# Kernel optimization log

Measured on AMD Instinct MI355X. Metric: run time of the kernel, lower is better.

## Reference

```python
import jax, jax.numpy as jnp
import numpy as np


def setup_inputs() -> dict:
    key = jax.random.key(0)
    k1, k2, k3, k4 = jax.random.split(key, 4)
    B, S, d_in, d_out = 4, 2048, 1024, 1024
    x = jax.random.normal(k1, (B, S, d_in), dtype=jnp.float32)
    # torch nn.Linear weight is [d_out, d_in]; we store transposed [d_in, d_out]
    Wq = jax.random.normal(k2, (d_in, d_out), dtype=jnp.float32) * (1.0 / np.sqrt(d_in))
    Wk = jax.random.normal(k3, (d_in, d_out), dtype=jnp.float32) * (1.0 / np.sqrt(d_in))
    Wv = jax.random.normal(k4, (d_in, d_out), dtype=jnp.float32) * (1.0 / np.sqrt(d_in))
    return {"x": x, "Wq": Wq, "Wk": Wk, "Wv": Wv}


def reference(x, Wq, Wk, Wv):
    # x: [B, S, d_in]
    B, S, d_in = x.shape
    q = jnp.einsum("bsd,de->bse", x, Wq)
    k = jnp.einsum("bsd,de->bse", x, Wk)
    v = jnp.einsum("bsd,de->bse", x, Wv)
    scores = jnp.einsum("bqe,bke->bqk", q, k)  # [B, S, S]
    causal = jnp.triu(jnp.ones((S, S), dtype=bool), k=1)  # True above diagonal
    scores = jnp.where(causal[None, :, :], -jnp.inf, scores)
    # NOTE: original scales by sqrt(d_in), not sqrt(d_out)
    scale = jnp.asarray(1.0 / np.sqrt(d_in), dtype=scores.dtype)
    weights = jax.nn.softmax(scores * scale, axis=-1)
    # dropout p=0.0 -> identity
    return jnp.einsum("bqk,bke->bqe", weights, v)
```

## Files before the change

kernel.cpp:

```cpp
#include <hip/hip_runtime.h>
#include <hip/hip_bf16.h>

typedef __attribute__((ext_vector_type(8))) short short8;
typedef __attribute__((ext_vector_type(4))) float f32x4;
typedef unsigned short ushort_t;

__device__ __forceinline__ ushort_t f2bf(float f) {
    union { __hip_bfloat16 h; ushort_t u; } c;
    c.h = __float2bfloat16(f);
    return c.u;
}

__device__ __forceinline__ void gload16(const ushort_t* g, ushort_t* l) {
    __builtin_amdgcn_global_load_lds(
        (const __attribute__((address_space(1))) void*)g,
        (__attribute__((address_space(3))) void*)l, 16, 0, 0);
}

__global__ __launch_bounds__(256) void k_convert_x(const float* __restrict__ x,
                                                   ushort_t* __restrict__ xb) {
    size_t idx = ((size_t)blockIdx.x * 256 + threadIdx.x) * 8;
    float4 a = *(const float4*)(x + idx);
    float4 b = *(const float4*)(x + idx + 4);
    short8 o;
    o[0] = (short)f2bf(a.x); o[1] = (short)f2bf(a.y);
    o[2] = (short)f2bf(a.z); o[3] = (short)f2bf(a.w);
    o[4] = (short)f2bf(b.x); o[5] = (short)f2bf(b.y);
    o[6] = (short)f2bf(b.z); o[7] = (short)f2bf(b.w);
    *(short8*)(xb + idx) = o;
}

__global__ __launch_bounds__(256) void k_transpose_w(const float* __restrict__ W0,
                                                     const float* __restrict__ W1,
                                                     const float* __restrict__ W2,
                                                     ushort_t* __restrict__ Wt) {
    const float* W = (blockIdx.z == 0) ? W0 : (blockIdx.z == 1) ? W1 : W2;
    ushort_t* out = Wt + (size_t)blockIdx.z * 1024 * 1024;
    __shared__ float tile[32][33];
    int tx = threadIdx.x, ty = threadIdx.y;
    int d0 = blockIdx.y * 32, e0 = blockIdx.x * 32;
#pragma unroll
    for (int i = 0; i < 32; i += 8)
        tile[ty + i][tx] = W[(size_t)(d0 + ty + i) * 1024 + e0 + tx];
    __syncthreads();
#pragma unroll
    for (int i = 0; i < 32; i += 8)
        out[(size_t)(e0 + ty + i) * 1024 + d0 + tx] = f2bf(tile[tx][ty + i]);
}

__global__ __launch_bounds__(256) void k_transpose_v(const ushort_t* __restrict__ V,
                                                     ushort_t* __restrict__ Vt) {
    int b = blockIdx.z;
    const ushort_t* in = V + (size_t)b * 2048 * 1024;
    ushort_t* out = Vt + (size_t)b * 1024 * 2048;
    __shared__ ushort_t tile[32][33];
    int tx = threadIdx.x, ty = threadIdx.y;
    int e0 = blockIdx.x * 32, j0 = blockIdx.y * 32;
#pragma unroll
    for (int i = 0; i < 32; i += 8)
        tile[ty + i][tx] = in[(size_t)(j0 + ty + i) * 1024 + e0 + tx];
    __syncthreads();
#pragma unroll
    for (int i = 0; i < 32; i += 8)
        out[(size_t)(e0 + ty + i) * 2048 + j0 + tx] = tile[tx][ty + i];
}

__global__ __launch_bounds__(512) void k_proj256(const ushort_t* __restrict__ X,
                                                 const ushort_t* __restrict__ Wt,
                                                 ushort_t* __restrict__ QKV) {
    const int bm = blockIdx.x, bn = blockIdx.y;

    __shared__ ushort_t Asm[2][16384];
    __shared__ ushort_t Bsm[2][16384];

    const int tid = threadIdx.x;
    const int l = tid & 63, w = tid >> 6;
    const int wrow = w >> 2, wcol = w & 3;
    const int lr = l & 15, lg = l >> 4;
    const int cx = (lr & 7) << 3;

    const int srow = tid >> 3;
    const int scol = (((tid & 7) ^ (srow & 7)) << 3);
    const ushort_t* Ag = X  + (size_t)(bm * 256 + srow) * 1024 + scol;
    const ushort_t* Bg = Wt + (size_t)(bn * 256 + srow) * 1024 + scol;

    f32x4 zero = {0.f, 0.f, 0.f, 0.f};
    f32x4 acc[8][4];
#pragma unroll
    for (int m = 0; m < 8; ++m)
#pragma unroll
        for (int n = 0; n < 4; ++n) acc[m][n] = zero;

    auto stageA = [&](int T) {
        ushort_t* dst = &Asm[T & 1][tid * 8];
        const ushort_t* src = Ag + T * 64;
#pragma unroll
        for (int c = 0; c < 4; ++c)
            gload16(src + (size_t)(c * 64) * 1024, dst + c * 4096);
    };
    auto stageB = [&](int T) {
        ushort_t* dst = &Bsm[T & 1][tid * 8];
        const ushort_t* src = Bg + T * 64;
#pragma unroll
        for (int c = 0; c < 4; ++c)
            gload16(src + (size_t)(c * 64) * 1024, dst + c * 4096);
    };

    stageA(0); stageB(0);
    asm volatile("s_waitcnt vmcnt(0)" ::: "memory");
    __builtin_amdgcn_s_barrier();

    for (int T = 0; T < 16; ++T) {
        const ushort_t* As = Asm[T & 1];
        const ushort_t* Bs = Bsm[T & 1];
        short8 a[4][2], b[4][2];

        if (T + 1 < 16) stageA(T + 1);
#pragma unroll
        for (int nf = 0; nf < 4; ++nf)
#pragma unroll
            for (int kh = 0; kh < 2; ++kh)
                b[nf][kh] = *(const short8*)&Bs[(wcol * 64 + nf * 16 + lr) * 64 + ((kh * 32 + lg * 8) ^ cx)];
#pragma unroll
        for (int mf = 0; mf < 4; ++mf)
#pragma unroll
            for (int kh = 0; kh < 2; ++kh)
                a[mf][kh] = *(const short8*)&As[(wrow * 128 + mf * 16 + lr) * 64 + ((kh * 32 + lg * 8) ^ cx)];
        __builtin_amdgcn_s_setprio(1);
#pragma unroll
        for (int mf = 0; mf < 4; ++mf)
#pragma unroll
            for (int nf = 0; nf < 2; ++nf)
#pragma unroll
                for (int kh = 0; kh < 2; ++kh)
                    acc[mf][nf] = __builtin_amdgcn_mfma_f32_16x16x32_bf16(a[mf][kh], b[nf][kh], acc[mf][nf], 0, 0, 0);
        __builtin_amdgcn_s_setprio(0);
        __builtin_amdgcn_s_barrier();

        if (T + 1 < 16) stageB(T + 1);
        __builtin_amdgcn_s_setprio(1);
#pragma unroll
        for (int mf = 0; mf < 4; ++mf)
#pragma unroll
            for (int nf = 2; nf < 4; ++nf)
#pragma unroll
                for (int kh = 0; kh < 2; ++kh)
                    acc[mf][nf] = __builtin_amdgcn_mfma_f32_16x16x32_bf16(a[mf][kh], b[nf][kh], acc[mf][nf], 0, 0, 0);
        __builtin_amdgcn_s_setprio(0);
        __builtin_amdgcn_s_barrier();

#pragma unroll
        for (int mf = 0; mf < 4; ++mf)
#pragma unroll
            for (int kh = 0; kh < 2; ++kh)
                a[mf][kh] = *(const short8*)&As[(wrow * 128 + 64 + mf * 16 + lr) * 64 + ((kh * 32 + lg * 8) ^ cx)];
        __builtin_amdgcn_s_setprio(1);
#pragma unroll
        for (int mf = 0; mf < 4; ++mf)
#pragma unroll
            for (int nf = 0; nf < 2; ++nf)
#pragma unroll
                for (int kh = 0; kh < 2; ++kh)
                    acc[4 + mf][nf] = __builtin_amdgcn_mfma_f32_16x16x32_bf16(a[mf][kh], b[nf][kh], acc[4 + mf][nf], 0, 0, 0);
        __builtin_amdgcn_s_setprio(0);
        __builtin_amdgcn_s_barrier();

        __builtin_amdgcn_s_setprio(1);
#pragma unroll
        for (int mf = 0; mf < 4; ++mf)
#pragma unroll
            for (int nf = 2; nf < 4; ++nf)
#pragma unroll
                for (int kh = 0; kh < 2; ++kh)
                    acc[4 + mf][nf] = __builtin_amdgcn_mfma_f32_16x16x32_bf16(a[mf][kh], b[nf][kh], acc[4 + mf][nf], 0, 0, 0);
        __builtin_amdgcn_s_setprio(0);
        asm volatile("s_waitcnt vmcnt(0)" ::: "memory");
        __builtin_amdgcn_s_barrier();
    }

    ushort_t* C = QKV + (size_t)(bn >> 2) * 8388608;
    const int colbase = (bn & 3) * 256 + wcol * 64;
    const int rb = lg * 4;
#pragma unroll
    for (int m = 0; m < 8; ++m)
#pragma unroll
        for (int nf = 0; nf < 4; ++nf) {
            int col = colbase + nf * 16 + lr;
#pragma unroll
            for (int r = 0; r < 4; ++r) {
                int grow = bm * 256 + wrow * 128 + m * 16 + rb + r;
                C[(size_t)grow * 1024 + col] = f2bf(acc[m][nf][r]);
            }
        }
}

template <int MODE>
__global__ __launch_bounds__(256) void k_gemm(const ushort_t* __restrict__ Abase,
                                              const ushort_t* __restrict__ Bbase,
                                              void* __restrict__ Cbase) {
    const int bz = blockIdx.z;
    int bm, bn;
    const ushort_t* A;
    const ushort_t* B;
    int lda, ldb, nk;
    if constexpr (MODE == 1) {
        int x = blockIdx.x;
        bm = (int)((sqrtf(8.f * x + 1.f) - 1.f) * 0.5f);
        while ((bm + 1) * (bm + 2) / 2 <= x) ++bm;
        while (bm * (bm + 1) / 2 > x) --bm;
        bn = x - bm * (bm + 1) / 2;
        A = Abase + (size_t)bz * 2048 * 1024; lda = 1024;
        B = Bbase + (size_t)bz * 2048 * 1024; ldb = 1024;
        nk = 32;
    } else {
        int xr = blockIdx.x;
        bm = (xr & 1) ? (15 - (xr >> 1)) : (xr >> 1);
        bn = blockIdx.y;
        A = Abase + (size_t)bz * 2048 * 4096; lda = 4096;
        B = Bbase + (size_t)bz * 1024 * 2048; ldb = 2048;
        nk = (bm + 1) * 4;
    }

    __shared__ ushort_t As[128 * 32];
    __shared__ ushort_t Bs[128 * 32];

    const int tid = threadIdx.x;
    const int l = tid & 63, wid = tid >> 6;
    const int wr = (wid >> 1) * 64, wc = (wid & 1) * 64;
    const int lr = l & 15, kc = (l >> 4) * 8;

    const int srow = tid >> 2, skb = (tid & 3) * 8;
    const ushort_t* ag = A + (size_t)(bm * 128 + srow) * lda + skb;
    const ushort_t* bg = B + (size_t)(bn * 128 + srow) * ldb + skb;
    const size_t a64 = (size_t)64 * lda, b64 = (size_t)64 * ldb;
    ushort_t* al = As + tid * 8;
    ushort_t* bl = Bs + tid * 8;

    f32x4 zero = {0.f, 0.f, 0.f, 0.f};
    f32x4 acc[4][4];
#pragma unroll
    for (int m = 0; m < 4; ++m)
#pragma unroll
        for (int n = 0; n < 4; ++n) acc[m][n] = zero;

    for (int ks = 0; ks < nk; ++ks) {
        __syncthreads();
        gload16(ag, al);
        gload16(ag + a64, al + 2048);
        gload16(bg, bl);
        gload16(bg + b64, bl + 2048);
        ag += 32; bg += 32;
        __syncthreads();

        short8 a[4], b[4];
#pragma unroll
        for (int m = 0; m < 4; ++m)
            a[m] = *(const short8*)&As[(wr + m * 16 + lr) * 32 + kc];
#pragma unroll
        for (int n = 0; n < 4; ++n)
            b[n] = *(const short8*)&Bs[(wc + n * 16 + lr) * 32 + kc];
#pragma unroll
        for (int m = 0; m < 4; ++m)
#pragma unroll
            for (int n = 0; n < 4; ++n)
                acc[m][n] = __builtin_amdgcn_mfma_f32_16x16x32_bf16(a[m], b[n], acc[m][n], 0, 0, 0);
    }

    const int rbase = (l >> 4) * 4;
    const int cbase = l & 15;
#pragma unroll
    for (int m = 0; m < 4; ++m) {
#pragma unroll
        for (int n = 0; n < 4; ++n) {
            int row0 = wr + m * 16 + rbase;
            int col = wc + n * 16 + cbase;
            int gcol = bn * 128 + col;
#pragma unroll
            for (int r = 0; r < 4; ++r) {
                int grow = bm * 128 + row0 + r;
                float v = acc[m][n][r];
                if constexpr (MODE == 1) {
                    float* C = (float*)Cbase + (size_t)bz * 2048 * 2048;
                    if (gcol <= grow) C[(size_t)grow * 2048 + gcol] = v * 0.03125f;
                } else {
                    float* C = (float*)Cbase + (size_t)bz * 2048 * 1024;
                    C[(size_t)grow * 1024 + gcol] = v;
                }
            }
        }
    }
}

__global__ __launch_bounds__(256) void k_softmax(float* __restrict__ scores) {
    const int t = blockIdx.x;
    const int i = t & 2047;
    const int limit = ((i >> 7) + 1) << 7;
    float* row = scores + (size_t)t * 2048;
    const int tid = threadIdx.x;
    const int j0 = tid * 8;
    const bool active = (j0 < limit);

    float v[8];
    if (active) {
        float4 f0 = *(const float4*)(row + j0);
        float4 f1 = *(const float4*)(row + j0 + 4);
        v[0] = f0.x; v[1] = f0.y; v[2] = f0.z; v[3] = f0.w;
        v[4] = f1.x; v[5] = f1.y; v[6] = f1.z; v[7] = f1.w;
    }

    float m = -3.0e38f;
    if (active) {
#pragma unroll
        for (int e = 0; e < 8; ++e)
            if (j0 + e <= i) m = fmaxf(m, v[e]);
    }
#pragma unroll
    for (int off = 32; off > 0; off >>= 1) m = fmaxf(m, __shfl_down(m, off, 64));

    __shared__ float redm[4];
    __shared__ float reds[4];
    const int lane = tid & 63, wid = tid >> 6;
    if (lane == 0) redm[wid] = m;
    __syncthreads();
    m = fmaxf(fmaxf(redm[0], redm[1]), fmaxf(redm[2], redm[3]));

    float p[8];
    float s = 0.f;
    if (active) {
#pragma unroll
        for (int e = 0; e < 8; ++e) {
            p[e] = (j0 + e <= i) ? __expf(v[e] - m) : 0.f;
            s += p[e];
        }
    }
#pragma unroll
    for (int off = 32; off > 0; off >>= 1) s += __shfl_down(s, off, 64);
    if (lane == 0) reds[wid] = s;
    __syncthreads();
    s = reds[0] + reds[1] + reds[2] + reds[3];
    float inv = 1.f / s;

    if (active) {
        short8 o;
#pragma unroll
        for (int e = 0; e < 8; ++e) o[e] = (short)f2bf(p[e] * inv);
        *(short8*)((ushort_t*)row + j0) = o;
    }
}

extern "C" void kernel_launch(void* const* d_in, const int* in_sizes, int n_in,
                              void* d_out, int out_size, void* d_ws, size_t ws_size,
                              hipStream_t stream) {
    const float* x  = (const float*)d_in[0];
    const float* Wq = (const float*)d_in[1];
    const float* Wk = (const float*)d_in[2];
    const float* Wv = (const float*)d_in[3];

    char* ws = (char*)d_ws;
    ushort_t* xb     = (ushort_t*)(ws);
    ushort_t* Wt     = (ushort_t*)(ws + 16777216);
    ushort_t* QKV    = (ushort_t*)(ws + 23068672);
    ushort_t* Vt     = (ushort_t*)(ws + 73400320);
    float*    scores = (float*)   (ws + 90177536);

    ushort_t* Q = QKV;
    ushort_t* K = QKV + (size_t)8192 * 1024;
    ushort_t* V = QKV + (size_t)2 * 8192 * 1024;

    k_convert_x<<<4096, 256, 0, stream>>>(x, xb);
    k_transpose_w<<<dim3(32, 32, 3), dim3(32, 8), 0, stream>>>(Wq, Wk, Wv, Wt);
    k_proj256<<<dim3(32, 12), 512, 0, stream>>>(xb, Wt, QKV);
    k_transpose_v<<<dim3(32, 64, 4), dim3(32, 8), 0, stream>>>(V, Vt);
    k_gemm<1><<<dim3(136, 1, 4), 256, 0, stream>>>(Q, K, scores);
    k_softmax<<<8192, 256, 0, stream>>>(scores);
    k_gemm<2><<<dim3(16, 8, 4), 256, 0, stream>>>((const ushort_t*)scores, Vt, (float*)d_out);
}
```

Before: 204.2 us.

## Pipeline projection GEMM at half-tile granularity with deeper prefetch

Splits the shared-memory A/B tiles of the QKV projection GEMM into half-tiles and stages them at finer granularity. Each half-tile load is issued between MFMA phases, with the A half for step t+2 prefetched early, and the full vmcnt(0) drain is replaced by vmcnt(2). Warps now read from their own half-tile, and the loop is unrolled by 2 with explicit LDS waits and scheduling barriers. The goal is to overlap global-to-LDS traffic with matrix math and cut stalls at barriers. In exchange it adds more barriers and relies on delicate waitcnt accounting, where a miscount could race.

```diff
diff --git a/kernel.cpp b/kernel.cpp
--- a/kernel.cpp
+++ b/kernel.cpp
@@ -16,6 +16,8 @@
         (const __attribute__((address_space(1))) void*)g,
         (__attribute__((address_space(3))) void*)l, 16, 0, 0);
 }
+
+#define FENCE asm volatile("" ::: "memory")
 
 __global__ __launch_bounds__(256) void k_convert_x(const float* __restrict__ x,
                                                    ushort_t* __restrict__ xb) {
@@ -70,8 +72,8 @@
                                                  ushort_t* __restrict__ QKV) {
     const int bm = blockIdx.x, bn = blockIdx.y;
 
-    __shared__ ushort_t Asm[2][16384];
-    __shared__ ushort_t Bsm[2][16384];
+    __shared__ ushort_t Asm[2][2][8192];
+    __shared__ ushort_t Bsm[2][2][8192];
 
     const int tid = threadIdx.x;
     const int l = tid & 63, w = tid >> 6;
@@ -81,8 +83,21 @@
 
     const int srow = tid >> 3;
     const int scol = (((tid & 7) ^ (srow & 7)) << 3);
-    const ushort_t* Ag = X  + (size_t)(bm * 256 + srow) * 1024 + scol;
-    const ushort_t* Bg = Wt + (size_t)(bn * 256 + srow) * 1024 + scol;
+    const ushort_t* Ags = X  + (size_t)(bm * 256 + srow) * 1024 + scol;
+    const ushort_t* Bgs = Wt + (size_t)(bn * 256 + srow) * 1024 + scol;
+
+    auto stageA = [&](int T, int hf) {
+        const ushort_t* src = Ags + (size_t)(hf * 128) * 1024 + T * 64;
+        ushort_t* dst = &Asm[T & 1][hf][tid * 8];
+        gload16(src, dst);
+        gload16(src + (size_t)64 * 1024, dst + 4096);
+    };
+    auto stageB = [&](int T, int hf) {
+        const ushort_t* src = Bgs + (size_t)(hf * 128) * 1024 + T * 64;
+        ushort_t* dst = &Bsm[T & 1][hf][tid * 8];
+        gload16(src, dst);
+        gload16(src + (size_t)64 * 1024, dst + 4096);
+    };
 
     f32x4 zero = {0.f, 0.f, 0.f, 0.f};
     f32x4 acc[8][4];
@@ -91,41 +106,33 @@
 #pragma unroll
         for (int n = 0; n < 4; ++n) acc[m][n] = zero;
 
-    auto stageA = [&](int T) {
-        ushort_t* dst = &Asm[T & 1][tid * 8];
-        const ushort_t* src = Ag + T * 64;
-#pragma unroll
-        for (int c = 0; c < 4; ++c)
-            gload16(src + (size_t)(c * 64) * 1024, dst + c * 4096);
-    };
-    auto stageB = [&](int T) {
-        ushort_t* dst = &Bsm[T & 1][tid * 8];
-        const ushort_t* src = Bg + T * 64;
-#pragma unroll
-        for (int c = 0; c < 4; ++c)
-            gload16(src + (size_t)(c * 64) * 1024, dst + c * 4096);
-    };
-
-    stageA(0); stageB(0);
-    asm volatile("s_waitcnt vmcnt(0)" ::: "memory");
+    stageA(0, 0); stageB(0, 0); stageA(0, 1); stageB(0, 1); stageA(1, 0);
+    asm volatile("s_waitcnt vmcnt(2)" ::: "memory");
     __builtin_amdgcn_s_barrier();
 
-    for (int T = 0; T < 16; ++T) {
-        const ushort_t* As = Asm[T & 1];
-        const ushort_t* Bs = Bsm[T & 1];
-        short8 a[4][2], b[4][2];
-
-        if (T + 1 < 16) stageA(T + 1);
-#pragma unroll
-        for (int nf = 0; nf < 4; ++nf)
+    const int brow = (wcol & 1) * 64;
+
+#pragma unroll 2
+    for (int t = 0; t < 16; ++t) {
+        const int db = t & 1;
+        const ushort_t* Ah = Asm[db][wrow];
+        const ushort_t* Bh = Bsm[db][wcol >> 1];
+        short8 a[4][2], b0[2][2], b1[2][2];
+
+#pragma unroll
+        for (int mf = 0; mf < 4; ++mf)
 #pragma unroll
             for (int kh = 0; kh < 2; ++kh)
-                b[nf][kh] = *(const short8*)&Bs[(wcol * 64 + nf * 16 + lr) * 64 + ((kh * 32 + lg * 8) ^ cx)];
-#pragma unroll
-        for (int mf = 0; mf < 4; ++mf)
+                a[mf][kh] = *(const short8*)&Ah[(mf * 16 + lr) * 64 + ((kh * 32 + lg * 8) ^ cx)];
+#pragma unroll
+        for (int nf = 0; nf < 2; ++nf)
 #pragma unroll
             for (int kh = 0; kh < 2; ++kh)
-                a[mf][kh] = *(const short8*)&As[(wrow * 128 + mf * 16 + lr) * 64 + ((kh * 32 + lg * 8) ^ cx)];
+                b0[nf][kh] = *(const short8*)&Bh[(brow + nf * 16 + lr) * 64 + ((kh * 32 + lg * 8) ^ cx)];
+        if (t < 15) stageB(t + 1, 0);
+        FENCE; __builtin_amdgcn_s_barrier();
+        asm volatile("s_waitcnt lgkmcnt(0)" ::: "memory");
+        __builtin_amdgcn_sched_barrier(0);
         __builtin_amdgcn_s_setprio(1);
 #pragma unroll
         for (int mf = 0; mf < 4; ++mf)
@@ -133,27 +140,39 @@
             for (int nf = 0; nf < 2; ++nf)
 #pragma unroll
                 for (int kh = 0; kh < 2; ++kh)
-                    acc[mf][nf] = __builtin_amdgcn_mfma_f32_16x16x32_bf16(a[mf][kh], b[nf][kh], acc[mf][nf], 0, 0, 0);
+                    acc[mf][nf] = __builtin_amdgcn_mfma_f32_16x16x32_bf16(a[mf][kh], b0[nf][kh], acc[mf][nf], 0, 0, 0);
         __builtin_amdgcn_s_setprio(0);
-        __builtin_amdgcn_s_barrier();
-
-        if (T + 1 < 16) stageB(T + 1);
+        FENCE; __builtin_amdgcn_s_barrier(); FENCE;
+
+#pragma unroll
+        for (int nf = 0; nf < 2; ++nf)
+#pragma unroll
+            for (int kh = 0; kh < 2; ++kh)
+                b1[nf][kh] = *(const short8*)&Bh[(brow + (nf + 2) * 16 + lr) * 64 + ((kh * 32 + lg * 8) ^ cx)];
+        if (t < 15) stageA(t + 1, 1);
+        FENCE; __builtin_amdgcn_s_barrier();
+        asm volatile("s_waitcnt lgkmcnt(0)" ::: "memory");
+        __builtin_amdgcn_sched_barrier(0);
         __builtin_amdgcn_s_setprio(1);
 #pragma unroll
         for (int mf = 0; mf < 4; ++mf)
 #pragma unroll
-            for (int nf = 2; nf < 4; ++nf)
+            for (int nf = 0; nf < 2; ++nf)
 #pragma unroll
                 for (int kh = 0; kh < 2; ++kh)
-                    acc[mf][nf] = __builtin_amdgcn_mfma_f32_16x16x32_bf16(a[mf][kh], b[nf][kh], acc[mf][nf], 0, 0, 0);
+                    acc[mf][nf + 2] = __builtin_amdgcn_mfma_f32_16x16x32_bf16(a[mf][kh], b1[nf][kh], acc[mf][nf + 2], 0, 0, 0);
         __builtin_amdgcn_s_setprio(0);
-        __builtin_amdgcn_s_barrier();
+        FENCE; __builtin_amdgcn_s_barrier(); FENCE;
 
 #pragma unroll
         for (int mf = 0; mf < 4; ++mf)
 #pragma unroll
             for (int kh = 0; kh < 2; ++kh)
-                a[mf][kh] = *(const short8*)&As[(wrow * 128 + 64 + mf * 16 + lr) * 64 + ((kh * 32 + lg * 8) ^ cx)];
+                a[mf][kh] = *(const short8*)&Ah[(64 + mf * 16 + lr) * 64 + ((kh * 32 + lg * 8) ^ cx)];
+        if (t < 15) stageB(t + 1, 1);
+        FENCE; __builtin_amdgcn_s_barrier();
+        asm volatile("s_waitcnt lgkmcnt(0)" ::: "memory");
+        __builtin_amdgcn_sched_barrier(0);
         __builtin_amdgcn_s_setprio(1);
 #pragma unroll
         for (int mf = 0; mf < 4; ++mf)
@@ -161,21 +180,29 @@
             for (int nf = 0; nf < 2; ++nf)
 #pragma unroll
                 for (int kh = 0; kh < 2; ++kh)
-                    acc[4 + mf][nf] = __builtin_amdgcn_mfma_f32_16x16x32_bf16(a[mf][kh], b[nf][kh], acc[4 + mf][nf], 0, 0, 0);
+                    acc[4 + mf][nf] = __builtin_amdgcn_mfma_f32_16x16x32_bf16(a[mf][kh], b0[nf][kh], acc[4 + mf][nf], 0, 0, 0);
         __builtin_amdgcn_s_setprio(0);
-        __builtin_amdgcn_s_barrier();
-
+        FENCE; __builtin_amdgcn_s_barrier(); FENCE;
+
+        if (t < 14) stageA(t + 2, 0);
+        FENCE; __builtin_amdgcn_s_barrier();
+        asm volatile("s_waitcnt lgkmcnt(0)" ::: "memory");
+        __builtin_amdgcn_sched_barrier(0);
         __builtin_amdgcn_s_setprio(1);
 #pragma unroll
         for (int mf = 0; mf < 4; ++mf)
 #pragma unroll
-            for (int nf = 2; nf < 4; ++nf)
+            for (int nf = 0; nf < 2; ++nf)
 #pragma unroll
                 for (int kh = 0; kh < 2; ++kh)
-                    acc[4 + mf][nf] = __builtin_amdgcn_mfma_f32_16x16x32_bf16(a[mf][kh], b[nf][kh], acc[4 + mf][nf], 0, 0, 0);
+                    acc[4 + mf][nf + 2] = __builtin_amdgcn_mfma_f32_16x16x32_bf16(a[mf][kh], b1[nf][kh], acc[4 + mf][nf + 2], 0, 0, 0);
         __builtin_amdgcn_s_setprio(0);
-        asm volatile("s_waitcnt vmcnt(0)" ::: "memory");
-        __builtin_amdgcn_s_barrier();
+        if (t < 14) {
+            asm volatile("s_waitcnt vmcnt(2)" ::: "memory");
+        } else if (t == 14) {
+            asm volatile("s_waitcnt vmcnt(0)" ::: "memory");
+        }
+        FENCE; __builtin_amdgcn_s_barrier(); FENCE;
     }
 
     ushort_t* C = QKV + (size_t)(bn >> 2) * 8388608;
```

Result: no change. 200.3 us (-2.0%).
